# Performance work log

Measured on AMD Instinct MI355X. Metric: run time of the kernel, lower is better.

The kernel has to match this reference:

```python
import jax, jax.numpy as jnp
import numpy as np

NUM_NODES = 100000
NUM_FEATURES = 64
HIDDEN = 128
NUM_CLASSES = 2
N_CLIQUES = 500000
CLIQUE_SIZE = 4


def setup_inputs() -> dict:
    key = jax.random.key(0)
    k = jax.random.split(key, 8)
    x = jax.random.normal(k[0], (NUM_NODES, NUM_FEATURES), dtype=jnp.float32)
    cliques_r = jax.random.randint(k[1], (N_CLIQUES, CLIQUE_SIZE), 0, NUM_NODES)
    cliques_s = jax.random.randint(k[2], (N_CLIQUES, CLIQUE_SIZE), 0, NUM_NODES)
    # learned parameters
    node_features = jax.random.normal(k[3], (NUM_NODES, NUM_FEATURES), dtype=jnp.float32)
    W5 = jax.random.normal(k[4], (NUM_FEATURES, HIDDEN), dtype=jnp.float32) / np.sqrt(NUM_FEATURES)
    b5 = jnp.zeros((HIDDEN,), dtype=jnp.float32)
    W6 = jax.random.normal(k[5], (HIDDEN, NUM_CLASSES), dtype=jnp.float32) / np.sqrt(HIDDEN)
    b6 = jnp.zeros((NUM_CLASSES,), dtype=jnp.float32)
    return {"x": x, "cliques_r": cliques_r, "cliques_s": cliques_s,
            "node_features": node_features, "W5": W5, "b5": b5, "W6": W6, "b6": b6}


def _edge_pred(node_features, cliques, W5, b5, W6, b6):
    # EdgePredNet: edge_index = positions 0..k-1, so x_i = clique node 0, x_j = clique node 1.
    x_i = node_features[cliques[:, 0]]  # [N, F] irregular gather
    x_j = node_features[cliques[:, 1]]  # [N, F]
    h = jax.nn.relu((x_i * x_j) @ W5 + b5)  # [N, H]
    logits = h @ W6 + b6  # [N, C]
    return jax.nn.softmax(logits, axis=-1)


def reference(x, cliques_r, cliques_s, node_features, W5, b5, W6, b6):
    # forward ignores the x argument: x = self.node_features
    probs_r = _edge_pred(node_features, cliques_r, W5, b5, W6, b6)           # [Nr, C]
    probs_s = _edge_pred(node_features, cliques_s, W5, b5, W6, b6)[:, None]  # [Ns, 1, C] (stacked singleton lists)
    return probs_r, probs_s
```

## Files before the change

kernel.cpp:

```cpp
#include <hip/hip_runtime.h>
#include <hip/hip_fp16.h>

typedef _Float16 half8 __attribute__((ext_vector_type(8)));
typedef float    f32x4 __attribute__((ext_vector_type(4)));

#define NF        64
#define HID       128
#define NPAIRS    31250
#define RPAIRS    15625
#define NFH_ELEMS 6400000

__global__ __launch_bounds__(256) void cvt_kernel(const float* __restrict__ nf,
                                                  _Float16* __restrict__ nfh)
{
    const long id = (long)blockIdx.x * 256 + threadIdx.x;
    if (id >= NFH_ELEMS / 8) return;
    const float4 u = ((const float4*)nf)[id * 2 + 0];
    const float4 v = ((const float4*)nf)[id * 2 + 1];
    half8 h;
    h[0] = (_Float16)u.x; h[1] = (_Float16)u.y; h[2] = (_Float16)u.z; h[3] = (_Float16)u.w;
    h[4] = (_Float16)v.x; h[5] = (_Float16)v.y; h[6] = (_Float16)v.z; h[7] = (_Float16)v.w;
    ((half8*)nfh)[id] = h;
}

template <int PRE>
__global__ __launch_bounds__(256) void edge_pred_kernel(
    const float*    __restrict__ nf,
    const _Float16* __restrict__ nfh,
    const int*      __restrict__ cr,
    const int*      __restrict__ cs,
    const float*    __restrict__ w5,
    const float*    __restrict__ b5,
    const float*    __restrict__ w6,
    const float*    __restrict__ b6,
    float*          __restrict__ out)
{
    __shared__ _Float16 lfrag[16][64][8];

    const int tid  = threadIdx.x;
    const int lane = tid & 63;
    const int wid  = tid >> 6;
    const int i    = lane & 15;
    const int g    = lane >> 4;

    {
        const int l = tid & 63, fb = tid >> 6;
        const int li = l & 15, lg = l >> 4;
        for (int f = fb; f < 16; f += 4) {
            const int t = f >> 1, kb = f & 1;
            const int col = 16 * t + li;
            half8 v;
#pragma unroll
            for (int e = 0; e < 8; ++e)
                v[e] = (_Float16)w5[(32 * kb + 8 * lg + e) * HID + col];
            *(half8*)&lfrag[f][l][0] = v;
        }
    }
    __syncthreads();

    float b5r[8], wdr[8];
#pragma unroll
    for (int t = 0; t < 8; ++t) {
        const int col = 16 * t + i;
        b5r[t] = b5[col];
        wdr[t] = w6[2 * col] - w6[2 * col + 1];
    }
    const float bdiff = b6[0] - b6[1];

    const int gw = blockIdx.x * 4 + wid;
    const int nw = gridDim.x * 4;
    if (gw >= NPAIRS) return;

    auto clqpair = [&](int p, int2& c0, int2& c1) {
        p = (p < NPAIRS) ? p : (NPAIRS - 1);
        const int* cl  = (p < RPAIRS) ? cr : cs;
        const long e0  = (long)((p < RPAIRS) ? p : p - RPAIRS) * 32 + i;
        c0 = *(const int2*)(cl + e0 * 4);
        c1 = *(const int2*)(cl + (e0 + 16) * 4);
    };
    auto gather1 = [&](int2 ix, half8& x0, half8& x1, half8& y0, half8& y1) {
        if constexpr (PRE) {
            const _Float16* p0 = nfh + (long)ix.x * NF;
            const _Float16* p1 = nfh + (long)ix.y * NF;
            x0 = *(const half8*)(p0 + 8 * g);
            x1 = *(const half8*)(p0 + 32 + 8 * g);
            y0 = *(const half8*)(p1 + 8 * g);
            y1 = *(const half8*)(p1 + 32 + 8 * g);
        } else {
            const float* p0 = nf + (long)ix.x * NF;
            const float* p1 = nf + (long)ix.y * NF;
            const float4 a = *(const float4*)(p0 + 8 * g);
            const float4 b = *(const float4*)(p0 + 8 * g + 4);
            const float4 c = *(const float4*)(p0 + 32 + 8 * g);
            const float4 d = *(const float4*)(p0 + 32 + 8 * g + 4);
            const float4 e = *(const float4*)(p1 + 8 * g);
            const float4 f = *(const float4*)(p1 + 8 * g + 4);
            const float4 m = *(const float4*)(p1 + 32 + 8 * g);
            const float4 n = *(const float4*)(p1 + 32 + 8 * g + 4);
            x0[0]=(_Float16)a.x; x0[1]=(_Float16)a.y; x0[2]=(_Float16)a.z; x0[3]=(_Float16)a.w;
            x0[4]=(_Float16)b.x; x0[5]=(_Float16)b.y; x0[6]=(_Float16)b.z; x0[7]=(_Float16)b.w;
            x1[0]=(_Float16)c.x; x1[1]=(_Float16)c.y; x1[2]=(_Float16)c.z; x1[3]=(_Float16)c.w;
            x1[4]=(_Float16)d.x; x1[5]=(_Float16)d.y; x1[6]=(_Float16)d.z; x1[7]=(_Float16)d.w;
            y0[0]=(_Float16)e.x; y0[1]=(_Float16)e.y; y0[2]=(_Float16)e.z; y0[3]=(_Float16)e.w;
            y0[4]=(_Float16)f.x; y0[5]=(_Float16)f.y; y0[6]=(_Float16)f.z; y0[7]=(_Float16)f.w;
            y1[0]=(_Float16)m.x; y1[1]=(_Float16)m.y; y1[2]=(_Float16)m.z; y1[3]=(_Float16)m.w;
            y1[4]=(_Float16)n.x; y1[5]=(_Float16)n.y; y1[6]=(_Float16)n.z; y1[7]=(_Float16)n.w;
        }
    };

    int2 ix0, ix1, ixn0, ixn1;
    half8 d[8];
    clqpair(gw, ix0, ix1);
    gather1(ix0, d[0], d[1], d[2], d[3]);
    gather1(ix1, d[4], d[5], d[6], d[7]);
    clqpair(gw + nw, ixn0, ixn1);

    for (int p = gw; p < NPAIRS; p += nw) {
        const half8 a00 = d[0] * d[2];
        const half8 a01 = d[1] * d[3];
        const half8 a10 = d[4] * d[6];
        const half8 a11 = d[5] * d[7];

        gather1(ixn0, d[0], d[1], d[2], d[3]);
        gather1(ixn1, d[4], d[5], d[6], d[7]);
        clqpair(p + 2 * nw, ixn0, ixn1);

        float su[2][4] = {{0.f,0.f,0.f,0.f},{0.f,0.f,0.f,0.f}};
#pragma unroll
        for (int t = 0; t < 8; ++t) {
            const half8 bf0 = *(const half8*)&lfrag[2 * t + 0][lane][0];
            const half8 bf1 = *(const half8*)&lfrag[2 * t + 1][lane][0];
            f32x4 z0 = {0.f,0.f,0.f,0.f}, z1 = {0.f,0.f,0.f,0.f};
            z0 = __builtin_amdgcn_mfma_f32_16x16x32_f16(a00, bf0, z0, 0, 0, 0);
            z0 = __builtin_amdgcn_mfma_f32_16x16x32_f16(a01, bf1, z0, 0, 0, 0);
            z1 = __builtin_amdgcn_mfma_f32_16x16x32_f16(a10, bf0, z1, 0, 0, 0);
            z1 = __builtin_amdgcn_mfma_f32_16x16x32_f16(a11, bf1, z1, 0, 0, 0);
#pragma unroll
            for (int r = 0; r < 4; ++r) {
                const float h0 = fmaxf(z0[r] + b5r[t], 0.f);
                const float h1 = fmaxf(z1[r] + b5r[t], 0.f);
                su[0][r] = fmaf(h0, wdr[t], su[0][r]);
                su[1][r] = fmaf(h1, wdr[t], su[1][r]);
            }
        }

#pragma unroll
        for (int u = 0; u < 2; ++u)
#pragma unroll
            for (int r = 0; r < 4; ++r) {
                float a_ = su[u][r];
                a_ += __shfl_xor(a_, 1);
                a_ += __shfl_xor(a_, 2);
                a_ += __shfl_xor(a_, 4);
                a_ += __shfl_xor(a_, 8);
                su[u][r] = a_;
            }

        if (i < 8) {
            const int r = i >> 1, c = i & 1;
#pragma unroll
            for (int u = 0; u < 2; ++u) {
                const float sv = (r == 0) ? su[u][0] : (r == 1) ? su[u][1]
                               : (r == 2) ? su[u][2] : su[u][3];
                const float z  = sv + bdiff;
                const float pz = 1.0f / (1.0f + __expf(-z));
                const long tile = 2L * p + u;
                out[tile * 32 + 8 * g + i] = c ? (1.0f - pz) : pz;
            }
        }
    }
}

extern "C" void kernel_launch(void* const* d_in, const int* in_sizes, int n_in,
                              void* d_out, int out_size, void* d_ws, size_t ws_size,
                              hipStream_t stream) {
    const float* nf = (const float*)d_in[3];
    const int*   cr = (const int*)d_in[1];
    const int*   cs = (const int*)d_in[2];
    const float* w5 = (const float*)d_in[4];
    const float* b5 = (const float*)d_in[5];
    const float* w6 = (const float*)d_in[6];
    const float* b6 = (const float*)d_in[7];
    float* out = (float*)d_out;

    if (ws_size >= (size_t)NFH_ELEMS * 2) {
        _Float16* nfh = (_Float16*)d_ws;
        hipLaunchKernelGGL(cvt_kernel, dim3(NFH_ELEMS / 8 / 256), dim3(256), 0, stream,
                           nf, nfh);
        hipLaunchKernelGGL((edge_pred_kernel<1>), dim3(1024), dim3(256), 0, stream,
                           nf, nfh, cr, cs, w5, b5, w6, b6, out);
    } else {
        hipLaunchKernelGGL((edge_pred_kernel<0>), dim3(1024), dim3(256), 0, stream,
                           nf, (const _Float16*)nullptr, cr, cs, w5, b5, w6, b6, out);
    }
}
```

Measured before the change: 56.81 us.

## Deepen gather prefetch to two stages and move bias/W6 diff to LDS

```diff
diff --git a/kernel.cpp b/kernel.cpp
--- a/kernel.cpp
+++ b/kernel.cpp
@@ -36,6 +36,7 @@
     float*          __restrict__ out)
 {
     __shared__ _Float16 lfrag[16][64][8];
+    __shared__ float2   bwl[8][16];
 
     const int tid  = threadIdx.x;
     const int lane = tid & 63;
@@ -55,16 +56,14 @@
                 v[e] = (_Float16)w5[(32 * kb + 8 * lg + e) * HID + col];
             *(half8*)&lfrag[f][l][0] = v;
         }
+        if (tid < 128) {
+            const int t = tid >> 4, ii = tid & 15;
+            const int col = 16 * t + ii;
+            bwl[t][ii] = make_float2(b5[col], w6[2 * col] - w6[2 * col + 1]);
+        }
     }
     __syncthreads();
 
-    float b5r[8], wdr[8];
-#pragma unroll
-    for (int t = 0; t < 8; ++t) {
-        const int col = 16 * t + i;
-        b5r[t] = b5[col];
-        wdr[t] = w6[2 * col] - w6[2 * col + 1];
-    }
     const float bdiff = b6[0] - b6[1];
 
     const int gw = blockIdx.x * 4 + wid;
@@ -92,7 +91,7 @@
             const float4 a = *(const float4*)(p0 + 8 * g);
             const float4 b = *(const float4*)(p0 + 8 * g + 4);
             const float4 c = *(const float4*)(p0 + 32 + 8 * g);
-            const float4 d = *(const float4*)(p0 + 32 + 8 * g + 4);
+            const float4 dd= *(const float4*)(p0 + 32 + 8 * g + 4);
             const float4 e = *(const float4*)(p1 + 8 * g);
             const float4 f = *(const float4*)(p1 + 8 * g + 4);
             const float4 m = *(const float4*)(p1 + 32 + 8 * g);
@@ -100,7 +99,7 @@
             x0[0]=(_Float16)a.x; x0[1]=(_Float16)a.y; x0[2]=(_Float16)a.z; x0[3]=(_Float16)a.w;
             x0[4]=(_Float16)b.x; x0[5]=(_Float16)b.y; x0[6]=(_Float16)b.z; x0[7]=(_Float16)b.w;
             x1[0]=(_Float16)c.x; x1[1]=(_Float16)c.y; x1[2]=(_Float16)c.z; x1[3]=(_Float16)c.w;
-            x1[4]=(_Float16)d.x; x1[5]=(_Float16)d.y; x1[6]=(_Float16)d.z; x1[7]=(_Float16)d.w;
+            x1[4]=(_Float16)dd.x;x1[5]=(_Float16)dd.y;x1[6]=(_Float16)dd.z;x1[7]=(_Float16)dd.w;
             y0[0]=(_Float16)e.x; y0[1]=(_Float16)e.y; y0[2]=(_Float16)e.z; y0[3]=(_Float16)e.w;
             y0[4]=(_Float16)f.x; y0[5]=(_Float16)f.y; y0[6]=(_Float16)f.z; y0[7]=(_Float16)f.w;
             y1[0]=(_Float16)m.x; y1[1]=(_Float16)m.y; y1[2]=(_Float16)m.z; y1[3]=(_Float16)m.w;
@@ -108,22 +107,16 @@
         }
     };
 
-    int2 ix0, ix1, ixn0, ixn1;
-    half8 d[8];
-    clqpair(gw, ix0, ix1);
-    gather1(ix0, d[0], d[1], d[2], d[3]);
-    gather1(ix1, d[4], d[5], d[6], d[7]);
-    clqpair(gw + nw, ixn0, ixn1);
-
-    for (int p = gw; p < NPAIRS; p += nw) {
-        const half8 a00 = d[0] * d[2];
-        const half8 a01 = d[1] * d[3];
-        const half8 a10 = d[4] * d[6];
-        const half8 a11 = d[5] * d[7];
-
-        gather1(ixn0, d[0], d[1], d[2], d[3]);
-        gather1(ixn1, d[4], d[5], d[6], d[7]);
-        clqpair(p + 2 * nw, ixn0, ixn1);
+    auto halfstep = [&](half8 (&D)[8], int2 iaU0, int2 iaU1,
+                        int2& ibF0, int2& ibF1, int p, int pidx_next) {
+        const half8 a00 = D[0] * D[2];
+        const half8 a01 = D[1] * D[3];
+        const half8 a10 = D[4] * D[6];
+        const half8 a11 = D[5] * D[7];
+
+        gather1(iaU0, D[0], D[1], D[2], D[3]);
+        gather1(iaU1, D[4], D[5], D[6], D[7]);
+        clqpair(pidx_next, ibF0, ibF1);
 
         float su[2][4] = {{0.f,0.f,0.f,0.f},{0.f,0.f,0.f,0.f}};
 #pragma unroll
@@ -135,12 +128,13 @@
             z0 = __builtin_amdgcn_mfma_f32_16x16x32_f16(a01, bf1, z0, 0, 0, 0);
             z1 = __builtin_amdgcn_mfma_f32_16x16x32_f16(a10, bf0, z1, 0, 0, 0);
             z1 = __builtin_amdgcn_mfma_f32_16x16x32_f16(a11, bf1, z1, 0, 0, 0);
+            const float2 bw = bwl[t][i];
 #pragma unroll
             for (int r = 0; r < 4; ++r) {
-                const float h0 = fmaxf(z0[r] + b5r[t], 0.f);
-                const float h1 = fmaxf(z1[r] + b5r[t], 0.f);
-                su[0][r] = fmaf(h0, wdr[t], su[0][r]);
-                su[1][r] = fmaf(h1, wdr[t], su[1][r]);
+                const float h0 = fmaxf(z0[r] + bw.x, 0.f);
+                const float h1 = fmaxf(z1[r] + bw.x, 0.f);
+                su[0][r] = fmaf(h0, bw.y, su[0][r]);
+                su[1][r] = fmaf(h1, bw.y, su[1][r]);
             }
         }
 
@@ -168,7 +162,25 @@
                 out[tile * 32 + 8 * g + i] = c ? (1.0f - pz) : pz;
             }
         }
+    };
+
+    half8 d[8], e[8];
+    int2 ixd0, ixd1, ixe0, ixe1;
+    clqpair(gw, ixd0, ixd1);
+    gather1(ixd0, d[0], d[1], d[2], d[3]);
+    gather1(ixd1, d[4], d[5], d[6], d[7]);
+    clqpair(gw + nw, ixe0, ixe1);
+    gather1(ixe0, e[0], e[1], e[2], e[3]);
+    gather1(ixe1, e[4], e[5], e[6], e[7]);
+    clqpair(gw + 2 * nw, ixd0, ixd1);
+
+    int p = gw;
+    for (; p + nw < NPAIRS; p += 2 * nw) {
+        halfstep(d, ixd0, ixd1, ixe0, ixe1, p, p + 3 * nw);
+        halfstep(e, ixe0, ixe1, ixd0, ixd1, p + nw, p + 4 * nw);
     }
+    if (p < NPAIRS)
+        halfstep(d, ixd0, ixd1, ixe0, ixe1, p, p);
 }
 
 extern "C" void kernel_launch(void* const* d_in, const int* in_sizes, int n_in,
```

New measurement: 62.62 us. 10.2% more time.

## Compact clique index pairs in convert pass, move bias/weights to LDS, grow grid

Applied to the files above, without the earlier changes.

```diff
diff --git a/kernel.cpp b/kernel.cpp
--- a/kernel.cpp
+++ b/kernel.cpp
@@ -6,29 +6,43 @@
 
 #define NF        64
 #define HID       128
+#define NEDGE     1000000
 #define NPAIRS    31250
 #define RPAIRS    15625
 #define NFH_ELEMS 6400000
 
+template <int MODE>
 __global__ __launch_bounds__(256) void cvt_kernel(const float* __restrict__ nf,
-                                                  _Float16* __restrict__ nfh)
+                                                  const int*   __restrict__ cr,
+                                                  const int*   __restrict__ cs,
+                                                  _Float16*    __restrict__ nfh,
+                                                  int2*        __restrict__ cc)
 {
     const long id = (long)blockIdx.x * 256 + threadIdx.x;
-    if (id >= NFH_ELEMS / 8) return;
-    const float4 u = ((const float4*)nf)[id * 2 + 0];
-    const float4 v = ((const float4*)nf)[id * 2 + 1];
-    half8 h;
-    h[0] = (_Float16)u.x; h[1] = (_Float16)u.y; h[2] = (_Float16)u.z; h[3] = (_Float16)u.w;
-    h[4] = (_Float16)v.x; h[5] = (_Float16)v.y; h[6] = (_Float16)v.z; h[7] = (_Float16)v.w;
-    ((half8*)nfh)[id] = h;
+    const long NCHUNK = NFH_ELEMS / 8;
+    if (id < NCHUNK) {
+        const float4 u = ((const float4*)nf)[id * 2 + 0];
+        const float4 v = ((const float4*)nf)[id * 2 + 1];
+        half8 h;
+        h[0] = (_Float16)u.x; h[1] = (_Float16)u.y; h[2] = (_Float16)u.z; h[3] = (_Float16)u.w;
+        h[4] = (_Float16)v.x; h[5] = (_Float16)v.y; h[6] = (_Float16)v.z; h[7] = (_Float16)v.w;
+        ((half8*)nfh)[id] = h;
+    } else if (MODE >= 2) {
+        const long e = id - NCHUNK;
+        if (e < NEDGE) {
+            const int* src = (e < NEDGE / 2) ? (cr + e * 4) : (cs + (e - NEDGE / 2) * 4);
+            cc[e] = *(const int2*)src;
+        }
+    }
 }
 
-template <int PRE>
+template <int MODE>
 __global__ __launch_bounds__(256) void edge_pred_kernel(
     const float*    __restrict__ nf,
     const _Float16* __restrict__ nfh,
     const int*      __restrict__ cr,
     const int*      __restrict__ cs,
+    const int2*     __restrict__ cc,
     const float*    __restrict__ w5,
     const float*    __restrict__ b5,
     const float*    __restrict__ w6,
@@ -36,6 +50,7 @@
     float*          __restrict__ out)
 {
     __shared__ _Float16 lfrag[16][64][8];
+    __shared__ float2   bwl[8][16];
 
     const int tid  = threadIdx.x;
     const int lane = tid & 63;
@@ -55,16 +70,14 @@
                 v[e] = (_Float16)w5[(32 * kb + 8 * lg + e) * HID + col];
             *(half8*)&lfrag[f][l][0] = v;
         }
+        if (tid < 128) {
+            const int t = tid >> 4, ii = tid & 15;
+            const int col = 16 * t + ii;
+            bwl[t][ii] = make_float2(b5[col], w6[2 * col] - w6[2 * col + 1]);
+        }
     }
     __syncthreads();
 
-    float b5r[8], wdr[8];
-#pragma unroll
-    for (int t = 0; t < 8; ++t) {
-        const int col = 16 * t + i;
-        b5r[t] = b5[col];
-        wdr[t] = w6[2 * col] - w6[2 * col + 1];
-    }
     const float bdiff = b6[0] - b6[1];
 
     const int gw = blockIdx.x * 4 + wid;
@@ -73,13 +86,19 @@
 
     auto clqpair = [&](int p, int2& c0, int2& c1) {
         p = (p < NPAIRS) ? p : (NPAIRS - 1);
-        const int* cl  = (p < RPAIRS) ? cr : cs;
-        const long e0  = (long)((p < RPAIRS) ? p : p - RPAIRS) * 32 + i;
-        c0 = *(const int2*)(cl + e0 * 4);
-        c1 = *(const int2*)(cl + (e0 + 16) * 4);
+        if constexpr (MODE >= 2) {
+            const long e0 = (long)p * 32 + i;
+            c0 = cc[e0];
+            c1 = cc[e0 + 16];
+        } else {
+            const int* cl  = (p < RPAIRS) ? cr : cs;
+            const long e0  = (long)((p < RPAIRS) ? p : p - RPAIRS) * 32 + i;
+            c0 = *(const int2*)(cl + e0 * 4);
+            c1 = *(const int2*)(cl + (e0 + 16) * 4);
+        }
     };
     auto gather1 = [&](int2 ix, half8& x0, half8& x1, half8& y0, half8& y1) {
-        if constexpr (PRE) {
+        if constexpr (MODE >= 1) {
             const _Float16* p0 = nfh + (long)ix.x * NF;
             const _Float16* p1 = nfh + (long)ix.y * NF;
             x0 = *(const half8*)(p0 + 8 * g);
@@ -92,7 +111,7 @@
             const float4 a = *(const float4*)(p0 + 8 * g);
             const float4 b = *(const float4*)(p0 + 8 * g + 4);
             const float4 c = *(const float4*)(p0 + 32 + 8 * g);
-            const float4 d = *(const float4*)(p0 + 32 + 8 * g + 4);
+            const float4 dd= *(const float4*)(p0 + 32 + 8 * g + 4);
             const float4 e = *(const float4*)(p1 + 8 * g);
             const float4 f = *(const float4*)(p1 + 8 * g + 4);
             const float4 m = *(const float4*)(p1 + 32 + 8 * g);
@@ -100,7 +119,7 @@
             x0[0]=(_Float16)a.x; x0[1]=(_Float16)a.y; x0[2]=(_Float16)a.z; x0[3]=(_Float16)a.w;
             x0[4]=(_Float16)b.x; x0[5]=(_Float16)b.y; x0[6]=(_Float16)b.z; x0[7]=(_Float16)b.w;
             x1[0]=(_Float16)c.x; x1[1]=(_Float16)c.y; x1[2]=(_Float16)c.z; x1[3]=(_Float16)c.w;
-            x1[4]=(_Float16)d.x; x1[5]=(_Float16)d.y; x1[6]=(_Float16)d.z; x1[7]=(_Float16)d.w;
+            x1[4]=(_Float16)dd.x;x1[5]=(_Float16)dd.y;x1[6]=(_Float16)dd.z;x1[7]=(_Float16)dd.w;
             y0[0]=(_Float16)e.x; y0[1]=(_Float16)e.y; y0[2]=(_Float16)e.z; y0[3]=(_Float16)e.w;
             y0[4]=(_Float16)f.x; y0[5]=(_Float16)f.y; y0[6]=(_Float16)f.z; y0[7]=(_Float16)f.w;
             y1[0]=(_Float16)m.x; y1[1]=(_Float16)m.y; y1[2]=(_Float16)m.z; y1[3]=(_Float16)m.w;
@@ -135,12 +154,13 @@
             z0 = __builtin_amdgcn_mfma_f32_16x16x32_f16(a01, bf1, z0, 0, 0, 0);
             z1 = __builtin_amdgcn_mfma_f32_16x16x32_f16(a10, bf0, z1, 0, 0, 0);
             z1 = __builtin_amdgcn_mfma_f32_16x16x32_f16(a11, bf1, z1, 0, 0, 0);
+            const float2 bw = bwl[t][i];
 #pragma unroll
             for (int r = 0; r < 4; ++r) {
-                const float h0 = fmaxf(z0[r] + b5r[t], 0.f);
-                const float h1 = fmaxf(z1[r] + b5r[t], 0.f);
-                su[0][r] = fmaf(h0, wdr[t], su[0][r]);
-                su[1][r] = fmaf(h1, wdr[t], su[1][r]);
+                const float h0 = fmaxf(z0[r] + bw.x, 0.f);
+                const float h1 = fmaxf(z1[r] + bw.x, 0.f);
+                su[0][r] = fmaf(h0, bw.y, su[0][r]);
+                su[1][r] = fmaf(h1, bw.y, su[1][r]);
             }
         }
 
@@ -183,14 +203,26 @@
     const float* b6 = (const float*)d_in[7];
     float* out = (float*)d_out;
 
-    if (ws_size >= (size_t)NFH_ELEMS * 2) {
+    const size_t need_nfh = (size_t)NFH_ELEMS * 2;
+    const size_t need_cc  = need_nfh + (size_t)NEDGE * 8;
+
+    if (ws_size >= need_cc) {
         _Float16* nfh = (_Float16*)d_ws;
-        hipLaunchKernelGGL(cvt_kernel, dim3(NFH_ELEMS / 8 / 256), dim3(256), 0, stream,
-                           nf, nfh);
-        hipLaunchKernelGGL((edge_pred_kernel<1>), dim3(1024), dim3(256), 0, stream,
-                           nf, nfh, cr, cs, w5, b5, w6, b6, out);
+        int2*     cc  = (int2*)((char*)d_ws + need_nfh);
+        const long work = NFH_ELEMS / 8 + NEDGE;
+        hipLaunchKernelGGL((cvt_kernel<2>), dim3((work + 255) / 256), dim3(256), 0,
+                           stream, nf, cr, cs, nfh, cc);
+        hipLaunchKernelGGL((edge_pred_kernel<2>), dim3(1280), dim3(256), 0, stream,
+                           nf, nfh, cr, cs, cc, w5, b5, w6, b6, out);
+    } else if (ws_size >= need_nfh) {
+        _Float16* nfh = (_Float16*)d_ws;
+        hipLaunchKernelGGL((cvt_kernel<1>), dim3(NFH_ELEMS / 8 / 256), dim3(256), 0,
+                           stream, nf, cr, cs, nfh, (int2*)nullptr);
+        hipLaunchKernelGGL((edge_pred_kernel<1>), dim3(1280), dim3(256), 0, stream,
+                           nf, nfh, cr, cs, (const int2*)nullptr, w5, b5, w6, b6, out);
     } else {
-        hipLaunchKernelGGL((edge_pred_kernel<0>), dim3(1024), dim3(256), 0, stream,
-                           nf, (const _Float16*)nullptr, cr, cs, w5, b5, w6, b6, out);
+        hipLaunchKernelGGL((edge_pred_kernel<0>), dim3(1280), dim3(256), 0, stream,
+                           nf, (const _Float16*)nullptr, cr, cs, (const int2*)nullptr,
+                           w5, b5, w6, b6, out);
     }
 }
```

Result: slower. 71.12 us (+25.2%).

## Quantize node features to int8 with per-row log scales and precompute edge scale products

Applied to the files above, without the earlier changes.

```diff
diff --git a/kernel.cpp b/kernel.cpp
--- a/kernel.cpp
+++ b/kernel.cpp
@@ -2,40 +2,96 @@
 #include <hip/hip_fp16.h>
 
 typedef _Float16 half8 __attribute__((ext_vector_type(8)));
+typedef _Float16 half4 __attribute__((ext_vector_type(4)));
 typedef float    f32x4 __attribute__((ext_vector_type(4)));
 
-#define NF        64
-#define HID       128
-#define NPAIRS    31250
-#define RPAIRS    15625
-#define NFH_ELEMS 6400000
-
-__global__ __launch_bounds__(256) void cvt_kernel(const float* __restrict__ nf,
-                                                  _Float16* __restrict__ nfh)
+#define NF      64
+#define HID     128
+#define NNODES  100000
+#define NEDGE   1000000
+#define NPAIRS  31250
+
+#define SMIN    2.2f
+#define SMAXA   7.0f
+#define LOGR    0.0771637f
+#define INVLOGR 12.9594f
+#define QBASE   (SMIN / 127.0f)
+
+#define OFF_SCODE 6400000ul
+#define OFF_SPROD 6502400ul
+#define OFF_CC    8601600ul
+
+__global__ __launch_bounds__(256) void quant_kernel(const float* __restrict__ nf,
+                                                    signed char* __restrict__ nfq,
+                                                    unsigned char* __restrict__ scode)
 {
-    const long id = (long)blockIdx.x * 256 + threadIdx.x;
-    if (id >= NFH_ELEMS / 8) return;
-    const float4 u = ((const float4*)nf)[id * 2 + 0];
-    const float4 v = ((const float4*)nf)[id * 2 + 1];
-    half8 h;
-    h[0] = (_Float16)u.x; h[1] = (_Float16)u.y; h[2] = (_Float16)u.z; h[3] = (_Float16)u.w;
-    h[4] = (_Float16)v.x; h[5] = (_Float16)v.y; h[6] = (_Float16)v.z; h[7] = (_Float16)v.w;
-    ((half8*)nfh)[id] = h;
-}
-
-template <int PRE>
+    const int row  = blockIdx.x * 4 + (threadIdx.x >> 6);
+    const int lane = threadIdx.x & 63;
+    if (row >= NNODES) return;
+    const float x = nf[(long)row * NF + lane];
+    float a = fabsf(x);
+    a = fmaxf(a, __shfl_xor(a, 1));
+    a = fmaxf(a, __shfl_xor(a, 2));
+    a = fmaxf(a, __shfl_xor(a, 4));
+    a = fmaxf(a, __shfl_xor(a, 8));
+    a = fmaxf(a, __shfl_xor(a, 16));
+    a = fmaxf(a, __shfl_xor(a, 32));
+    const float acl = fminf(fmaxf(a, SMIN), SMAXA);
+    int code = (int)ceilf(__logf(acl / SMIN) * INVLOGR);
+    code = min(max(code, 0), 15);
+    const float inv_s = (1.0f / QBASE) * __expf(-(float)code * LOGR);
+    int q = __float2int_rn(x * inv_s);
+    q = min(max(q, -127), 127);
+    nfq[(long)row * NF + lane] = (signed char)q;
+    if (lane == 0) scode[row] = (unsigned char)code;
+}
+
+__global__ __launch_bounds__(256) void sprod_kernel(const int* __restrict__ cr,
+                                                    const int* __restrict__ cs,
+                                                    const unsigned char* __restrict__ scode,
+                                                    int2* __restrict__ cc,
+                                                    _Float16* __restrict__ sprod)
+{
+    __shared__ unsigned char scl[NNODES / 2];
+    const int tid = threadIdx.x;
+    const unsigned int* src = (const unsigned int*)scode;
+    for (int j = tid; j < NNODES / 8; j += 256) {
+        const unsigned int u0 = src[2 * j], u1 = src[2 * j + 1];
+        const unsigned int v0 = u0 | (u0 >> 4), v1 = u1 | (u1 >> 4);
+        const unsigned int p0 = (v0 & 0xFFu) | ((v0 >> 8) & 0xFF00u);
+        const unsigned int p1 = (v1 & 0xFFu) | ((v1 >> 8) & 0xFF00u);
+        ((unsigned int*)scl)[j] = p0 | (p1 << 16);
+    }
+    __syncthreads();
+
+    for (long e = (long)blockIdx.x * 256 + tid; e < NEDGE; e += 128l * 256) {
+        const int2 nn = (e < NEDGE / 2) ? *(const int2*)(cr + e * 4)
+                                        : *(const int2*)(cs + (e - NEDGE / 2) * 4);
+        cc[e] = nn;
+        const unsigned char b0 = scl[nn.x >> 1], b1 = scl[nn.y >> 1];
+        const int c0 = (nn.x & 1) ? (b0 >> 4) : (b0 & 0xF);
+        const int c1 = (nn.y & 1) ? (b1 >> 4) : (b1 & 0xF);
+        const float sp = (QBASE * QBASE) * __expf((float)(c0 + c1) * LOGR);
+        sprod[e] = (_Float16)sp;
+    }
+}
+
+template <int QMODE>
 __global__ __launch_bounds__(256) void edge_pred_kernel(
-    const float*    __restrict__ nf,
-    const _Float16* __restrict__ nfh,
-    const int*      __restrict__ cr,
-    const int*      __restrict__ cs,
-    const float*    __restrict__ w5,
-    const float*    __restrict__ b5,
-    const float*    __restrict__ w6,
-    const float*    __restrict__ b6,
-    float*          __restrict__ out)
+    const float*       __restrict__ nf,
+    const signed char* __restrict__ nfq,
+    const int2*        __restrict__ cc,
+    const _Float16*    __restrict__ sprod,
+    const int*         __restrict__ cr,
+    const int*         __restrict__ cs,
+    const float*       __restrict__ w5,
+    const float*       __restrict__ b5,
+    const float*       __restrict__ w6,
+    const float*       __restrict__ b6,
+    float*             __restrict__ out)
 {
     __shared__ _Float16 lfrag[16][64][8];
+    __shared__ float2   bwl[8][16];
 
     const int tid  = threadIdx.x;
     const int lane = tid & 63;
@@ -47,83 +103,94 @@
         const int l = tid & 63, fb = tid >> 6;
         const int li = l & 15, lg = l >> 4;
         for (int f = fb; f < 16; f += 4) {
-            const int t = f >> 1, kb = f & 1;
+            const int t = f >> 1, c = f & 1;
             const int col = 16 * t + li;
             half8 v;
 #pragma unroll
             for (int e = 0; e < 8; ++e)
-                v[e] = (_Float16)w5[(32 * kb + 8 * lg + e) * HID + col];
+                v[e] = (_Float16)w5[(16 * lg + 8 * c + e) * HID + col];
             *(half8*)&lfrag[f][l][0] = v;
         }
+        if (tid < 128) {
+            const int t = tid >> 4, ii = tid & 15;
+            const int col = 16 * t + ii;
+            bwl[t][ii] = make_float2(b5[col], w6[2 * col] - w6[2 * col + 1]);
+        }
     }
     __syncthreads();
 
-    float b5r[8], wdr[8];
-#pragma unroll
-    for (int t = 0; t < 8; ++t) {
-        const int col = 16 * t + i;
-        b5r[t] = b5[col];
-        wdr[t] = w6[2 * col] - w6[2 * col + 1];
-    }
     const float bdiff = b6[0] - b6[1];
-
     const int gw = blockIdx.x * 4 + wid;
     const int nw = gridDim.x * 4;
     if (gw >= NPAIRS) return;
 
     auto clqpair = [&](int p, int2& c0, int2& c1) {
         p = (p < NPAIRS) ? p : (NPAIRS - 1);
-        const int* cl  = (p < RPAIRS) ? cr : cs;
-        const long e0  = (long)((p < RPAIRS) ? p : p - RPAIRS) * 32 + i;
-        c0 = *(const int2*)(cl + e0 * 4);
-        c1 = *(const int2*)(cl + (e0 + 16) * 4);
-    };
-    auto gather1 = [&](int2 ix, half8& x0, half8& x1, half8& y0, half8& y1) {
-        if constexpr (PRE) {
-            const _Float16* p0 = nfh + (long)ix.x * NF;
-            const _Float16* p1 = nfh + (long)ix.y * NF;
-            x0 = *(const half8*)(p0 + 8 * g);
-            x1 = *(const half8*)(p0 + 32 + 8 * g);
-            y0 = *(const half8*)(p1 + 8 * g);
-            y1 = *(const half8*)(p1 + 32 + 8 * g);
+        const long e0 = (long)p * 32 + i;
+        c0 = cc[e0];
+        c1 = cc[e0 + 16];
+    };
+    auto gatherq = [&](int2 ix, int4& X, int4& Y) {
+        X = *(const int4*)(nfq + (long)ix.x * NF + 16 * g);
+        Y = *(const int4*)(nfq + (long)ix.y * NF + 16 * g);
+    };
+    auto mkfrag = [&](const int4& X, const int4& Y, half8& A0, half8& A1) {
+        union U { int4 v; signed char b[16]; };
+        U ux, uy; ux.v = X; uy.v = Y;
+#pragma unroll
+        for (int e = 0; e < 8; ++e) {
+            A0[e] = (_Float16)(short)((short)ux.b[e]     * (short)uy.b[e]);
+            A1[e] = (_Float16)(short)((short)ux.b[e + 8] * (short)uy.b[e + 8]);
+        }
+    };
+    auto mkfrag0 = [&](int2 ix, half8& A0, half8& A1) {
+        const float* p0 = nf + (long)ix.x * NF + 16 * g;
+        const float* p1 = nf + (long)ix.y * NF + 16 * g;
+#pragma unroll
+        for (int e = 0; e < 8; ++e) {
+            A0[e] = (_Float16)(p0[e] * p1[e]);
+            A1[e] = (_Float16)(p0[e + 8] * p1[e + 8]);
+        }
+    };
+
+    int2 ix0, ix1, ixn0, ixn1;
+    int4 dX0, dY0, dX1, dY1;
+    if constexpr (QMODE) {
+        clqpair(gw, ix0, ix1);
+        gatherq(ix0, dX0, dY0);
+        gatherq(ix1, dX1, dY1);
+        clqpair(gw + nw, ixn0, ixn1);
+    }
+
+    for (int p = gw; p < NPAIRS; p += nw) {
+        half8 a00, a01, a10, a11;
+        if constexpr (QMODE) {
+            mkfrag(dX0, dY0, a00, a01);
+            mkfrag(dX1, dY1, a10, a11);
+            gatherq(ixn0, dX0, dY0);
+            gatherq(ixn1, dX1, dY1);
+            clqpair(p + 2 * nw, ixn0, ixn1);
         } else {
-            const float* p0 = nf + (long)ix.x * NF;
-            const float* p1 = nf + (long)ix.y * NF;
-            const float4 a = *(const float4*)(p0 + 8 * g);
-            const float4 b = *(const float4*)(p0 + 8 * g + 4);
-            const float4 c = *(const float4*)(p0 + 32 + 8 * g);
-            const float4 d = *(const float4*)(p0 + 32 + 8 * g + 4);
-            const float4 e = *(const float4*)(p1 + 8 * g);
-            const float4 f = *(const float4*)(p1 + 8 * g + 4);
-            const float4 m = *(const float4*)(p1 + 32 + 8 * g);
-            const float4 n = *(const float4*)(p1 + 32 + 8 * g + 4);
-            x0[0]=(_Float16)a.x; x0[1]=(_Float16)a.y; x0[2]=(_Float16)a.z; x0[3]=(_Float16)a.w;
-            x0[4]=(_Float16)b.x; x0[5]=(_Float16)b.y; x0[6]=(_Float16)b.z; x0[7]=(_Float16)b.w;
-            x1[0]=(_Float16)c.x; x1[1]=(_Float16)c.y; x1[2]=(_Float16)c.z; x1[3]=(_Float16)c.w;
-            x1[4]=(_Float16)d.x; x1[5]=(_Float16)d.y; x1[6]=(_Float16)d.z; x1[7]=(_Float16)d.w;
-            y0[0]=(_Float16)e.x; y0[1]=(_Float16)e.y; y0[2]=(_Float16)e.z; y0[3]=(_Float16)e.w;
-            y0[4]=(_Float16)f.x; y0[5]=(_Float16)f.y; y0[6]=(_Float16)f.z; y0[7]=(_Float16)f.w;
-            y1[0]=(_Float16)m.x; y1[1]=(_Float16)m.y; y1[2]=(_Float16)m.z; y1[3]=(_Float16)m.w;
-            y1[4]=(_Float16)n.x; y1[5]=(_Float16)n.y; y1[6]=(_Float16)n.z; y1[7]=(_Float16)n.w;
-        }
-    };
-
-    int2 ix0, ix1, ixn0, ixn1;
-    half8 d[8];
-    clqpair(gw, ix0, ix1);
-    gather1(ix0, d[0], d[1], d[2], d[3]);
-    gather1(ix1, d[4], d[5], d[6], d[7]);
-    clqpair(gw + nw, ixn0, ixn1);
-
-    for (int p = gw; p < NPAIRS; p += nw) {
-        const half8 a00 = d[0] * d[2];
-        const half8 a01 = d[1] * d[3];
-        const half8 a10 = d[4] * d[6];
-        const half8 a11 = d[5] * d[7];
-
-        gather1(ixn0, d[0], d[1], d[2], d[3]);
-        gather1(ixn1, d[4], d[5], d[6], d[7]);
-        clqpair(p + 2 * nw, ixn0, ixn1);
+            int2 j0, j1;
+            const long e0 = (long)p * 32 + i;
+            j0 = (e0 < NEDGE/2) ? *(const int2*)(cr + e0 * 4) : *(const int2*)(cs + (e0 - NEDGE/2) * 4);
+            const long e1 = e0 + 16;
+            j1 = (e1 < NEDGE/2) ? *(const int2*)(cr + e1 * 4) : *(const int2*)(cs + (e1 - NEDGE/2) * 4);
+            mkfrag0(j0, a00, a01);
+            mkfrag0(j1, a10, a11);
+        }
+
+        float sp0[4], sp1[4];
+        if constexpr (QMODE) {
+            const _Float16* spp = sprod + (long)32 * p + 4 * g;
+            const half4 h0 = *(const half4*)(spp);
+            const half4 h1 = *(const half4*)(spp + 16);
+#pragma unroll
+            for (int r = 0; r < 4; ++r) { sp0[r] = (float)h0[r]; sp1[r] = (float)h1[r]; }
+        } else {
+#pragma unroll
+            for (int r = 0; r < 4; ++r) { sp0[r] = 1.f; sp1[r] = 1.f; }
+        }
 
         float su[2][4] = {{0.f,0.f,0.f,0.f},{0.f,0.f,0.f,0.f}};
 #pragma unroll
@@ -135,12 +202,13 @@
             z0 = __builtin_amdgcn_mfma_f32_16x16x32_f16(a01, bf1, z0, 0, 0, 0);
             z1 = __builtin_amdgcn_mfma_f32_16x16x32_f16(a10, bf0, z1, 0, 0, 0);
             z1 = __builtin_amdgcn_mfma_f32_16x16x32_f16(a11, bf1, z1, 0, 0, 0);
+            const float2 bw = bwl[t][i];
 #pragma unroll
             for (int r = 0; r < 4; ++r) {
-                const float h0 = fmaxf(z0[r] + b5r[t], 0.f);
-                const float h1 = fmaxf(z1[r] + b5r[t], 0.f);
-                su[0][r] = fmaf(h0, wdr[t], su[0][r]);
-                su[1][r] = fmaf(h1, wdr[t], su[1][r]);
+                const float h0 = fmaxf(fmaf(z0[r], sp0[r], bw.x), 0.f);
+                const float h1 = fmaxf(fmaf(z1[r], sp1[r], bw.x), 0.f);
+                su[0][r] = fmaf(h0, bw.y, su[0][r]);
+                su[1][r] = fmaf(h1, bw.y, su[1][r]);
             }
         }
 
@@ -183,14 +251,21 @@
     const float* b6 = (const float*)d_in[7];
     float* out = (float*)d_out;
 
-    if (ws_size >= (size_t)NFH_ELEMS * 2) {
-        _Float16* nfh = (_Float16*)d_ws;
-        hipLaunchKernelGGL(cvt_kernel, dim3(NFH_ELEMS / 8 / 256), dim3(256), 0, stream,
-                           nf, nfh);
+    const size_t need = OFF_CC + (size_t)NEDGE * 8;
+    if (ws_size >= need) {
+        signed char*   nfq   = (signed char*)d_ws;
+        unsigned char* scode = (unsigned char*)d_ws + OFF_SCODE;
+        _Float16*      sprod = (_Float16*)((char*)d_ws + OFF_SPROD);
+        int2*          cc    = (int2*)((char*)d_ws + OFF_CC);
+        hipLaunchKernelGGL(quant_kernel, dim3(NNODES / 4), dim3(256), 0, stream,
+                           nf, nfq, scode);
+        hipLaunchKernelGGL(sprod_kernel, dim3(128), dim3(256), 0, stream,
+                           cr, cs, scode, cc, sprod);
         hipLaunchKernelGGL((edge_pred_kernel<1>), dim3(1024), dim3(256), 0, stream,
-                           nf, nfh, cr, cs, w5, b5, w6, b6, out);
+                           nf, nfq, cc, sprod, cr, cs, w5, b5, w6, b6, out);
     } else {
         hipLaunchKernelGGL((edge_pred_kernel<0>), dim3(1024), dim3(256), 0, stream,
-                           nf, (const _Float16*)nullptr, cr, cs, w5, b5, w6, b6, out);
-    }
-}
+                           nf, (const signed char*)nullptr, (const int2*)nullptr,
+                           (const _Float16*)nullptr, cr, cs, w5, b5, w6, b6, out);
+    }
+}
```

After: 87.34 us. 1.54x slower.
